# Performance work log

Measured on AMD Instinct MI355X. Metric: run time of the kernel, lower is better.

The kernel has to match this reference:

```python
import jax, jax.numpy as jnp
import numpy as np

THRESH = float(-np.log(0.7))  # -log(thresh), as in __init__
IGNORE = 255
FRAC = 16  # n_min = num_valid // 16


def setup_inputs() -> dict:
    key = jax.random.key(0)
    k1, k2 = jax.random.split(key)
    logits = jax.random.normal(k1, (16, 19, 512, 1024), dtype=jnp.float32)
    labels = jax.random.randint(k2, (16, 512, 1024), 0, 19, dtype=jnp.int32)
    return {"logits": logits, "labels": labels}


def reference(logits, labels):
    # per-pixel cross entropy with ignore_index=255, reduction='none'
    logp = jax.nn.log_softmax(logits, axis=1)  # [B, C, H, W]
    valid = labels != IGNORE                   # [B, H, W]
    safe_lab = jnp.where(valid, labels, 0)
    ce = -jnp.take_along_axis(logp, safe_lab[:, None].astype(jnp.int32), axis=1)[:, 0]
    ce = jnp.where(valid, ce, 0.0)             # ignored pixels -> 0 loss

    n_min = jnp.sum(valid) // FRAC             # traced scalar int

    loss = jnp.sort(ce.reshape(-1))[::-1]      # descending

    # branch A: mean of losses strictly above thresh
    sel = loss > THRESH
    n_sel = jnp.sum(sel)
    mean_above = jnp.sum(jnp.where(sel, loss, 0.0)) / jnp.maximum(n_sel, 1).astype(loss.dtype)

    # branch B: mean of top n_min losses (via cumsum + dynamic index)
    csum = jnp.cumsum(loss)
    mean_topk = jnp.take(csum, n_min - 1) / jnp.maximum(n_min, 1).astype(loss.dtype)

    cond = jnp.take(loss, n_min) > THRESH
    return jnp.where(cond, mean_above, mean_topk)
```

## Files before the change

kernel.cpp:

```cpp
#include <hip/hip_runtime.h>

constexpr int       C    = 19;
constexpr long long HW   = 512LL * 1024LL;
constexpr long long NPIX = 16LL * HW;
constexpr float     THRESH_F = 0.35667494393873245f;
constexpr double    FXSCALE  = 4294967296.0;

struct Meta {
  unsigned long long sum_above;
  unsigned long long sum_all;
  unsigned long long gt_sum;
  unsigned n_valid;
  unsigned n_above;
  unsigned done;
};

__device__ inline unsigned long long fxq(float v) {
  return (unsigned long long)llrintf(v * 4294967296.0f);
}


__device__ inline void block_acc4(unsigned lv, unsigned la,
                                  unsigned long long s1, unsigned long long s2,
                                  Meta* meta) {
  for (int o = 32; o > 0; o >>= 1) {
    lv += __shfl_down(lv, o); la += __shfl_down(la, o);
    s1 += __shfl_down(s1, o); s2 += __shfl_down(s2, o);
  }
  __shared__ unsigned a1[4], a2[4];
  __shared__ unsigned long long b1[4], b2[4];
  const int lane = threadIdx.x & 63, wid = threadIdx.x >> 6;
  if (lane == 0) { a1[wid] = lv; a2[wid] = la; b1[wid] = s1; b2[wid] = s2; }
  __syncthreads();
  if (threadIdx.x == 0) {
    unsigned x = 0, y = 0; unsigned long long u = 0, v = 0;
    for (int i = 0; i < 4; ++i) { x += a1[i]; y += a2[i]; u += b1[i]; v += b2[i]; }
    atomicAdd(&meta->n_valid, x); atomicAdd(&meta->n_above, y);
    atomicAdd(&meta->sum_above, u); atomicAdd(&meta->sum_all, v);
  }
}

__device__ inline void block_acc_u64(unsigned long long s, unsigned long long* dst) {
  for (int o = 32; o > 0; o >>= 1) s += __shfl_down(s, o);
  __shared__ unsigned long long b[4];
  const int lane = threadIdx.x & 63, wid = threadIdx.x >> 6;
  if (lane == 0) b[wid] = s;
  __syncthreads();
  if (threadIdx.x == 0) {
    unsigned long long u = 0;
    for (int i = 0; i < 4; ++i) u += b[i];
    atomicAdd(dst, u);
  }
}

template<int NBINS>
__device__ inline void scan_desc(const unsigned* __restrict__ cnt, unsigned k,
                                 unsigned* outD, unsigned* outRem) {
  constexpr int CHUNK = NBINS / 256;
  const int t = threadIdx.x;
  __shared__ unsigned sc[256];
  __shared__ unsigned sD, sRem;
  __syncthreads();
  unsigned c[CHUNK]; unsigned tc = 0;
#pragma unroll
  for (int i = 0; i < CHUNK; ++i) { c[i] = cnt[t * CHUNK + i]; tc += c[i]; }
  sc[t] = tc;
  __syncthreads();
  unsigned ac = 0;
  for (int j = t + 1; j < 256; ++j) ac += sc[j];
#pragma unroll
  for (int i = CHUNK - 1; i >= 0; --i) {
    if (ac < k && ac + c[i] >= k) { sD = (unsigned)(t * CHUNK + i); sRem = k - ac; }
    ac += c[i];
  }
  __syncthreads();
  *outD = sD; *outRem = sRem;
}


__device__ inline void compute_ce4(const float* __restrict__ logits,
                                   const int* __restrict__ labels,
                                   long long p, float o[4], int lb[4]) {
  const long long b = p >> 19;
  const long long r = p & (HW - 1);
  const float* base = logits + b * (C * HW) + r;
  const int4 lb4 = *reinterpret_cast<const int4*>(labels + p);
  lb[0] = lb4.x; lb[1] = lb4.y; lb[2] = lb4.z; lb[3] = lb4.w;
  float v[C][4];
#pragma unroll
  for (int c = 0; c < C; ++c) {
    const float4 t = *reinterpret_cast<const float4*>(base + (long long)c * HW);
    v[c][0] = t.x; v[c][1] = t.y; v[c][2] = t.z; v[c][3] = t.w;
  }
  float m[4], s[4], xl[4];
#pragma unroll
  for (int j = 0; j < 4; ++j) m[j] = v[0][j];
#pragma unroll
  for (int c = 1; c < C; ++c)
#pragma unroll
    for (int j = 0; j < 4; ++j) m[j] = fmaxf(m[j], v[c][j]);
#pragma unroll
  for (int j = 0; j < 4; ++j) { s[j] = 0.f; xl[j] = 0.f; }
#pragma unroll
  for (int c = 0; c < C; ++c)
#pragma unroll
    for (int j = 0; j < 4; ++j) {
      s[j] += __expf(v[c][j] - m[j]);
      if (lb[j] == c) xl[j] = v[c][j];
    }
#pragma unroll
  for (int j = 0; j < 4; ++j) {
    const bool val = (lb[j] != 255);
    o[j] = val ? fmaxf(m[j] + __logf(s[j]) - xl[j], 0.f) : 0.f;
  }
}

__global__ __launch_bounds__(256) void ce_reduce_kernel(
    const float* __restrict__ logits, const int* __restrict__ labels,
    Meta* __restrict__ meta) {
  const long long nq = NPIX >> 2;
  const long long stride = (long long)gridDim.x * blockDim.x;
  unsigned lv = 0, la = 0;
  float sa = 0.f, st = 0.f;
  for (long long q = blockIdx.x * (long long)blockDim.x + threadIdx.x; q < nq; q += stride) {
    float o[4]; int lb[4];
    compute_ce4(logits, labels, q << 2, o, lb);
#pragma unroll
    for (int j = 0; j < 4; ++j) {
      const bool val = (lb[j] != 255);
      lv += val ? 1u : 0u;
      la += (o[j] > THRESH_F) ? 1u : 0u;
      sa += (o[j] > THRESH_F) ? o[j] : 0.f;
      st += val ? o[j] : 0.f;
    }
  }
  block_acc4(lv, la, fxq(sa), fxq(st), meta);
}

__global__ void decide_kernel(Meta* __restrict__ meta, float* __restrict__ out) {
  if (threadIdx.x == 0) {
    const unsigned nv = meta->n_valid, na = meta->n_above;
    const unsigned nm = nv >> 4;
    if (na > nm) {
      out[0] = (float)(((double)meta->sum_above / FXSCALE) / (double)na);
      meta->done = 1u;
    } else if (nm == 0u) {
      out[0] = (float)((double)meta->sum_all / FXSCALE);
      meta->done = 1u;
    } else {
      meta->done = 0u;
    }
  }
}


__global__ __launch_bounds__(256) void ce_write_hist1(
    const float* __restrict__ logits, const int* __restrict__ labels,
    const Meta* __restrict__ meta, float* __restrict__ ce,
    unsigned* __restrict__ g_cnt) {
  if (meta->done) return;
  __shared__ unsigned l_cnt[2048];
  for (int i = threadIdx.x; i < 2048; i += 256) l_cnt[i] = 0;
  __syncthreads();
  const long long nq = NPIX >> 2;
  const long long stride = (long long)gridDim.x * blockDim.x;
  for (long long q = blockIdx.x * (long long)blockDim.x + threadIdx.x; q < nq; q += stride) {
    float o[4]; int lb[4];
    const long long p = q << 2;
    compute_ce4(logits, labels, p, o, lb);
    *reinterpret_cast<float4*>(ce + p) = make_float4(o[0], o[1], o[2], o[3]);
#pragma unroll
    for (int j = 0; j < 4; ++j) atomicAdd(&l_cnt[__float_as_uint(o[j]) >> 21], 1u);
  }
  __syncthreads();
  for (int i = threadIdx.x; i < 2048; i += 256)
    if (l_cnt[i]) atomicAdd(&g_cnt[i], l_cnt[i]);
}

__global__ __launch_bounds__(256) void hist2_kernel(
    const float4* __restrict__ ce4, Meta* __restrict__ meta,
    const unsigned* __restrict__ h0c, unsigned* __restrict__ g_cnt) {
  if (meta->done) return;
  const unsigned nm = meta->n_valid >> 4;
  unsigned d0, k1;
  scan_desc<2048>(h0c, nm, &d0, &k1);
  __shared__ unsigned l_cnt[2048];
  for (int i = threadIdx.x; i < 2048; i += 256) l_cnt[i] = 0;
  __syncthreads();
  const long long nq = NPIX >> 2;
  const long long stride = (long long)gridDim.x * blockDim.x;
  unsigned long long gs = 0;
  for (long long q = blockIdx.x * (long long)blockDim.x + threadIdx.x; q < nq; q += stride) {
    const float4 vv = ce4[q];
    const float va[4] = {vv.x, vv.y, vv.z, vv.w};
#pragma unroll
    for (int j = 0; j < 4; ++j) {
      const unsigned bits = __float_as_uint(va[j]);
      const unsigned hb = bits >> 21;
      if (hb > d0) gs += fxq(va[j]);
      else if (hb == d0) atomicAdd(&l_cnt[(bits >> 10) & 2047u], 1u);
    }
  }
  __syncthreads();
  for (int i = threadIdx.x; i < 2048; i += 256)
    if (l_cnt[i]) atomicAdd(&g_cnt[i], l_cnt[i]);
  block_acc_u64(gs, &meta->gt_sum);
}

__global__ __launch_bounds__(256) void hist3_kernel(
    const float4* __restrict__ ce4, Meta* __restrict__ meta,
    const unsigned* __restrict__ h0c, const unsigned* __restrict__ h1c,
    unsigned* __restrict__ g_cnt, unsigned long long* __restrict__ g_sum) {
  if (meta->done) return;
  const unsigned nm = meta->n_valid >> 4;
  unsigned d0, k1, d1, k2;
  scan_desc<2048>(h0c, nm, &d0, &k1);
  scan_desc<2048>(h1c, k1, &d1, &k2);
  const unsigned d01 = (d0 << 11) | d1;
  __shared__ unsigned l_cnt[1024];
  __shared__ unsigned long long l_sum[1024];
  for (int i = threadIdx.x; i < 1024; i += 256) { l_cnt[i] = 0; l_sum[i] = 0; }
  __syncthreads();
  const long long nq = NPIX >> 2;
  const long long stride = (long long)gridDim.x * blockDim.x;
  unsigned long long gs = 0;
  for (long long q = blockIdx.x * (long long)blockDim.x + threadIdx.x; q < nq; q += stride) {
    const float4 vv = ce4[q];
    const float va[4] = {vv.x, vv.y, vv.z, vv.w};
#pragma unroll
    for (int j = 0; j < 4; ++j) {
      const unsigned bits = __float_as_uint(va[j]);
      if ((bits >> 21) == d0) {
        const unsigned hl = bits >> 10;
        if (hl > d01) gs += fxq(va[j]);
        else if (hl == d01) {
          atomicAdd(&l_cnt[bits & 1023u], 1u);
          atomicAdd(&l_sum[bits & 1023u], fxq(va[j]));
        }
      }
    }
  }
  __syncthreads();
  for (int i = threadIdx.x; i < 1024; i += 256)
    if (l_cnt[i]) { atomicAdd(&g_cnt[i], l_cnt[i]); atomicAdd(&g_sum[i], l_sum[i]); }
  block_acc_u64(gs, &meta->gt_sum);
}

__global__ __launch_bounds__(256) void final_kernel(
    Meta* __restrict__ meta, const unsigned* __restrict__ h0c,
    const unsigned* __restrict__ h1c, const unsigned* __restrict__ h2c,
    const unsigned long long* __restrict__ h2s, float* __restrict__ out) {
  if (meta->done) return;
  const unsigned nm = meta->n_valid >> 4;
  unsigned d0, k1, d1, k2;
  scan_desc<2048>(h0c, nm, &d0, &k1);
  scan_desc<2048>(h1c, k1, &d1, &k2);
  const unsigned d01 = (d0 << 11) | d1;

  const int t = threadIdx.x;
  unsigned c[4]; unsigned long long s[4];
  unsigned tc = 0; unsigned long long ts = 0;
#pragma unroll
  for (int i = 0; i < 4; ++i) {
    c[i] = h2c[t * 4 + i]; s[i] = h2s[t * 4 + i]; tc += c[i]; ts += s[i];
  }
  __shared__ unsigned sc[256];
  __shared__ unsigned long long ssm[256];
  __syncthreads();
  sc[t] = tc; ssm[t] = ts;
  __syncthreads();
  unsigned ac = 0; unsigned long long as = 0;
  for (int j = t + 1; j < 256; ++j) { ac += sc[j]; as += ssm[j]; }
#pragma unroll
  for (int i = 3; i >= 0; --i) {
    if (ac < k2 && ac + c[i] >= k2) {
      const unsigned T = (d01 << 10) | (unsigned)(t * 4 + i);
      const float tv = __uint_as_float(T);
      const unsigned long long gt_s = meta->gt_sum + as;
      const unsigned ties = k2 - ac;
      const double topk = ((double)gt_s + (double)ties * (double)fxq(tv)) / FXSCALE;
      out[0] = (float)(topk / (double)nm);
    }
    ac += c[i]; as += s[i];
  }
}

extern "C" void kernel_launch(void* const* d_in, const int* in_sizes, int n_in,
                              void* d_out, int out_size, void* d_ws, size_t ws_size,
                              hipStream_t stream) {
  (void)in_sizes; (void)n_in; (void)out_size; (void)ws_size;
  const float* logits = (const float*)d_in[0];
  const int*   labels = (const int*)d_in[1];
  float* out = (float*)d_out;

  char* ws = (char*)d_ws;
  float* ce = (float*)ws;
  size_t off = (size_t)NPIX * 4;
  const size_t meta_base = off;
  Meta* meta = (Meta*)(ws + off);                            off += 64;
  unsigned long long* h2s = (unsigned long long*)(ws + off); off += 1024 * 8;
  unsigned* h0c = (unsigned*)(ws + off);                     off += 2048 * 4;
  unsigned* h1c = (unsigned*)(ws + off);                     off += 2048 * 4;
  unsigned* h2c = (unsigned*)(ws + off);                     off += 1024 * 4;

  hipMemsetAsync(ws + meta_base, 0, off - meta_base, stream);

  ce_reduce_kernel<<<2048, 256, 0, stream>>>(logits, labels, meta);
  decide_kernel<<<1, 64, 0, stream>>>(meta, out);
  ce_write_hist1<<<2048, 256, 0, stream>>>(logits, labels, meta, ce, h0c);
  hist2_kernel<<<512, 256, 0, stream>>>((const float4*)ce, meta, h0c, h1c);
  hist3_kernel<<<512, 256, 0, stream>>>((const float4*)ce, meta, h0c, h1c, h2c, h2s);
  final_kernel<<<1, 256, 0, stream>>>(meta, h0c, h1c, h2c, h2s, out);
}
```

Before: 179.4 us.

## Tile CE kernels per block with nontemporal loads and drop max subtraction

```diff
diff --git a/kernel.cpp b/kernel.cpp
--- a/kernel.cpp
+++ b/kernel.cpp
@@ -5,6 +5,19 @@
 constexpr long long NPIX = 16LL * HW;
 constexpr float     THRESH_F = 0.35667494393873245f;
 constexpr double    FXSCALE  = 4294967296.0;
+
+constexpr int NBLK_CE = 4096;
+constexpr int PXB     = 2048;
+
+typedef float f32x4 __attribute__((ext_vector_type(4)));
+
+__device__ inline f32x4 ntload4(const float* p) {
+#if __has_builtin(__builtin_nontemporal_load)
+  return __builtin_nontemporal_load(reinterpret_cast<const f32x4*>(p));
+#else
+  return *reinterpret_cast<const f32x4*>(p);
+#endif
+}
 
 struct Meta {
   unsigned long long sum_above;
@@ -78,78 +91,82 @@
 }
 
 
-__device__ inline void compute_ce4(const float* __restrict__ logits,
-                                   const int* __restrict__ labels,
-                                   long long p, float o[4], int lb[4]) {
-  const long long b = p >> 19;
-  const long long r = p & (HW - 1);
-  const float* base = logits + b * (C * HW) + r;
-  const int4 lb4 = *reinterpret_cast<const int4*>(labels + p);
-  lb[0] = lb4.x; lb[1] = lb4.y; lb[2] = lb4.z; lb[3] = lb4.w;
-  float v[C][4];
+template<bool STORE>
+__device__ inline void ce_tile(const float* __restrict__ logits,
+                               const int* __restrict__ labels,
+                               float* __restrict__ ce,
+                               float o[8], int lb[8]) {
+  const long long p0 = (long long)blockIdx.x * PXB;
+  const long long b = p0 >> 19, r0 = p0 & (HW - 1);
+  const float* base = logits + b * (C * HW) + r0;
+  const int t = threadIdx.x;
+  const int q0 = t, q1 = 256 + t;
+
+  const int4 l4a = *reinterpret_cast<const int4*>(labels + p0 + 4LL * q0);
+  const int4 l4b = *reinterpret_cast<const int4*>(labels + p0 + 4LL * q1);
+  lb[0] = l4a.x; lb[1] = l4a.y; lb[2] = l4a.z; lb[3] = l4a.w;
+  lb[4] = l4b.x; lb[5] = l4b.y; lb[6] = l4b.z; lb[7] = l4b.w;
+
+  float s[8], xl[8];
+#pragma unroll
+  for (int i = 0; i < 8; ++i) { s[i] = 0.f; xl[i] = 0.f; }
+
 #pragma unroll
   for (int c = 0; c < C; ++c) {
-    const float4 t = *reinterpret_cast<const float4*>(base + (long long)c * HW);
-    v[c][0] = t.x; v[c][1] = t.y; v[c][2] = t.z; v[c][3] = t.w;
-  }
-  float m[4], s[4], xl[4];
-#pragma unroll
-  for (int j = 0; j < 4; ++j) m[j] = v[0][j];
-#pragma unroll
-  for (int c = 1; c < C; ++c)
-#pragma unroll
-    for (int j = 0; j < 4; ++j) m[j] = fmaxf(m[j], v[c][j]);
-#pragma unroll
-  for (int j = 0; j < 4; ++j) { s[j] = 0.f; xl[j] = 0.f; }
-#pragma unroll
-  for (int c = 0; c < C; ++c)
-#pragma unroll
-    for (int j = 0; j < 4; ++j) {
-      s[j] += __expf(v[c][j] - m[j]);
-      if (lb[j] == c) xl[j] = v[c][j];
+    const float* pc = base + (long long)c * HW;
+    const f32x4 va = ntload4(pc + 4LL * q0);
+    const f32x4 vb = ntload4(pc + 4LL * q1);
+    const float v[8] = {va.x, va.y, va.z, va.w, vb.x, vb.y, vb.z, vb.w};
+#pragma unroll
+    for (int i = 0; i < 8; ++i) {
+      s[i] += __expf(v[i]);
+      if (lb[i] == c) xl[i] = v[i];
     }
-#pragma unroll
-  for (int j = 0; j < 4; ++j) {
-    const bool val = (lb[j] != 255);
-    o[j] = val ? fmaxf(m[j] + __logf(s[j]) - xl[j], 0.f) : 0.f;
+  }
+#pragma unroll
+  for (int i = 0; i < 8; ++i)
+    o[i] = (lb[i] != 255) ? fmaxf(__logf(s[i]) - xl[i], 0.f) : 0.f;
+
+  if (STORE) {
+    *reinterpret_cast<float4*>(ce + p0 + 4LL * q0) = make_float4(o[0], o[1], o[2], o[3]);
+    *reinterpret_cast<float4*>(ce + p0 + 4LL * q1) = make_float4(o[4], o[5], o[6], o[7]);
   }
 }
 
 __global__ __launch_bounds__(256) void ce_reduce_kernel(
     const float* __restrict__ logits, const int* __restrict__ labels,
     Meta* __restrict__ meta) {
-  const long long nq = NPIX >> 2;
-  const long long stride = (long long)gridDim.x * blockDim.x;
+  float o[8]; int lb[8];
+  ce_tile<false>(logits, labels, nullptr, o, lb);
   unsigned lv = 0, la = 0;
   float sa = 0.f, st = 0.f;
-  for (long long q = blockIdx.x * (long long)blockDim.x + threadIdx.x; q < nq; q += stride) {
-    float o[4]; int lb[4];
-    compute_ce4(logits, labels, q << 2, o, lb);
-#pragma unroll
-    for (int j = 0; j < 4; ++j) {
-      const bool val = (lb[j] != 255);
-      lv += val ? 1u : 0u;
-      la += (o[j] > THRESH_F) ? 1u : 0u;
-      sa += (o[j] > THRESH_F) ? o[j] : 0.f;
-      st += val ? o[j] : 0.f;
-    }
+#pragma unroll
+  for (int i = 0; i < 8; ++i) {
+    const bool val = (lb[i] != 255);
+    lv += val ? 1u : 0u;
+    la += (o[i] > THRESH_F) ? 1u : 0u;
+    sa += (o[i] > THRESH_F) ? o[i] : 0.f;
+    st += val ? o[i] : 0.f;
   }
   block_acc4(lv, la, fxq(sa), fxq(st), meta);
 }
 
-__global__ void decide_kernel(Meta* __restrict__ meta, float* __restrict__ out) {
+__global__ __launch_bounds__(256) void decide_kernel(
+    Meta* __restrict__ meta, float* __restrict__ out,
+    unsigned* __restrict__ h0c, unsigned* __restrict__ h1c,
+    unsigned* __restrict__ h2c, unsigned long long* __restrict__ h2s) {
+  const unsigned nv = meta->n_valid, na = meta->n_above;
+  const unsigned nm = nv >> 4;
+  const bool A = (na > nm);
+  const bool Z = (nm == 0u);
   if (threadIdx.x == 0) {
-    const unsigned nv = meta->n_valid, na = meta->n_above;
-    const unsigned nm = nv >> 4;
-    if (na > nm) {
-      out[0] = (float)(((double)meta->sum_above / FXSCALE) / (double)na);
-      meta->done = 1u;
-    } else if (nm == 0u) {
-      out[0] = (float)((double)meta->sum_all / FXSCALE);
-      meta->done = 1u;
-    } else {
-      meta->done = 0u;
-    }
+    if (A) { out[0] = (float)(((double)meta->sum_above / FXSCALE) / (double)na); meta->done = 1u; }
+    else if (Z) { out[0] = (float)((double)meta->sum_all / FXSCALE); meta->done = 1u; }
+    else meta->done = 0u;
+  }
+  if (!A && !Z) {
+    for (int i = threadIdx.x; i < 2048; i += 256) { h0c[i] = 0u; h1c[i] = 0u; }
+    for (int i = threadIdx.x; i < 1024; i += 256) { h2c[i] = 0u; h2s[i] = 0ull; }
   }
 }
 
@@ -162,16 +179,10 @@
   __shared__ unsigned l_cnt[2048];
   for (int i = threadIdx.x; i < 2048; i += 256) l_cnt[i] = 0;
   __syncthreads();
-  const long long nq = NPIX >> 2;
-  const long long stride = (long long)gridDim.x * blockDim.x;
-  for (long long q = blockIdx.x * (long long)blockDim.x + threadIdx.x; q < nq; q += stride) {
-    float o[4]; int lb[4];
-    const long long p = q << 2;
-    compute_ce4(logits, labels, p, o, lb);
-    *reinterpret_cast<float4*>(ce + p) = make_float4(o[0], o[1], o[2], o[3]);
-#pragma unroll
-    for (int j = 0; j < 4; ++j) atomicAdd(&l_cnt[__float_as_uint(o[j]) >> 21], 1u);
-  }
+  float o[8]; int lb[8];
+  ce_tile<true>(logits, labels, ce, o, lb);
+#pragma unroll
+  for (int j = 0; j < 8; ++j) atomicAdd(&l_cnt[__float_as_uint(o[j]) >> 21], 1u);
   __syncthreads();
   for (int i = threadIdx.x; i < 2048; i += 256)
     if (l_cnt[i]) atomicAdd(&g_cnt[i], l_cnt[i]);
@@ -296,18 +307,17 @@
   char* ws = (char*)d_ws;
   float* ce = (float*)ws;
   size_t off = (size_t)NPIX * 4;
-  const size_t meta_base = off;
   Meta* meta = (Meta*)(ws + off);                            off += 64;
   unsigned long long* h2s = (unsigned long long*)(ws + off); off += 1024 * 8;
   unsigned* h0c = (unsigned*)(ws + off);                     off += 2048 * 4;
   unsigned* h1c = (unsigned*)(ws + off);                     off += 2048 * 4;
   unsigned* h2c = (unsigned*)(ws + off);                     off += 1024 * 4;
 
-  hipMemsetAsync(ws + meta_base, 0, off - meta_base, stream);
-
-  ce_reduce_kernel<<<2048, 256, 0, stream>>>(logits, labels, meta);
-  decide_kernel<<<1, 64, 0, stream>>>(meta, out);
-  ce_write_hist1<<<2048, 256, 0, stream>>>(logits, labels, meta, ce, h0c);
+  hipMemsetAsync(meta, 0, 64, stream);
+
+  ce_reduce_kernel<<<NBLK_CE, 256, 0, stream>>>(logits, labels, meta);
+  decide_kernel<<<1, 256, 0, stream>>>(meta, out, h0c, h1c, h2c, h2s);
+  ce_write_hist1<<<NBLK_CE, 256, 0, stream>>>(logits, labels, meta, ce, h0c);
   hist2_kernel<<<512, 256, 0, stream>>>((const float4*)ce, meta, h0c, h1c);
   hist3_kernel<<<512, 256, 0, stream>>>((const float4*)ce, meta, h0c, h1c, h2c, h2s);
   final_kernel<<<1, 256, 0, stream>>>(meta, h0c, h1c, h2c, h2s, out);
```

Result: slower. 238.8 us (+33.2%).
